# Kernel optimization log

Measured on AMD Instinct MI355X. Metric: run time of the kernel, lower is better.

The kernel has to match this reference:

```python
import jax, jax.numpy as jnp
import numpy as np

C = 256      # in_channels
CI = 128     # inter_channels = in_channels // 2
B, H, W = 16, 64, 64
EPS = 1e-5   # BatchNorm2d default eps


def conv1x1(x, w, b=None):
    # x: (b,c,h,w), w: (o,c) -> (b,o,h,w)
    out = jnp.einsum('bchw,oc->bohw', x, w)
    if b is not None:
        out = out + b[None, :, None, None]
    return out


def maxpool2x2(x):
    b, c, h, w = x.shape
    return x.reshape(b, c, h // 2, 2, w // 2, 2).max(axis=(3, 5))


def setup_inputs() -> dict:
    key = jax.random.key(0)
    ks = jax.random.split(key, 12)
    s_in = 1.0 / np.sqrt(C)
    s_int = 1.0 / np.sqrt(CI)
    return {
        'x': jax.random.normal(ks[0], (B, C, H, W), jnp.float32),
        'y': jax.random.normal(ks[1], (B, C, H, W), jnp.float32),
        'theta_w': jax.random.uniform(ks[2], (CI, C), jnp.float32, -s_in, s_in),
        'theta_b': jax.random.uniform(ks[3], (CI,), jnp.float32, -s_in, s_in),
        'phi_w': jax.random.uniform(ks[4], (CI, C), jnp.float32, -s_in, s_in),
        'phi_b': jax.random.uniform(ks[5], (CI,), jnp.float32, -s_in, s_in),
        'g_w': jax.random.uniform(ks[6], (CI, C), jnp.float32, -s_in, s_in),
        'g_b': jax.random.uniform(ks[7], (CI,), jnp.float32, -s_in, s_in),
        'W_w': jax.random.uniform(ks[8], (C, CI), jnp.float32, -s_int, s_int),
        'W_b': jax.random.uniform(ks[9], (C,), jnp.float32, -s_int, s_int),
        'bn_gamma': jax.random.normal(ks[10], (C,), jnp.float32) * 0.1,
        'bn_beta': jax.random.normal(ks[11], (C,), jnp.float32) * 0.1,
    }


def reference(x, y, theta_w, theta_b, phi_w, phi_b, g_w, g_b, W_w, W_b, bn_gamma, bn_beta):
    b, c, h, w = x.shape
    # g branch: 1x1 conv on y + 2x2 maxpool -> (b, CI, hw/4) -> (b, hw/4, CI)
    g_y = maxpool2x2(conv1x1(y, g_w, g_b)).reshape(b, CI, -1).transpose(0, 2, 1)
    # theta branch: 1x1 conv on x -> (b, hw, CI)
    theta_x = conv1x1(x, theta_w, theta_b).reshape(b, CI, -1).transpose(0, 2, 1)
    # phi branch: 1x1 conv on y + maxpool -> (b, CI, hw/4)
    phi_y = maxpool2x2(conv1x1(y, phi_w, phi_b)).reshape(b, CI, -1)
    # attention: (b, hw, hw/4)
    f = jnp.einsum('bnc,bcm->bnm', theta_x, phi_y)
    f_div_C = jax.nn.softmax(f, axis=-1)
    # z: (b, hw, CI) -> (b, CI, h, w)
    z = jnp.einsum('bnm,bmc->bnc', f_div_C, g_y)
    z = z.transpose(0, 2, 1).reshape(b, CI, h, w)
    # W: 1x1 conv + BatchNorm2d (training-mode batch stats, biased var)
    wz = conv1x1(z, W_w, W_b)
    mean = wz.mean(axis=(0, 2, 3), keepdims=True)
    var = wz.var(axis=(0, 2, 3), keepdims=True)
    wz = (wz - mean) * jax.lax.rsqrt(var + EPS)
    wz = wz * bn_gamma[None, :, None, None] + bn_beta[None, :, None, None]
    return wz + x
```

## Files before the change

kernel.cpp:

```cpp
#include <hip/hip_runtime.h>
#include <cstdint>

#define HW 4096
#define NC 256
#define CI 128
#define NB 16
#define MP 1024

typedef __bf16 bfv8 __attribute__((ext_vector_type(8)));
typedef float f32x16 __attribute__((ext_vector_type(16)));

__device__ __forceinline__ uint32_t bfr(float x) {
    uint32_t u = __float_as_uint(x);
    return (u + 0x7fffu + ((u >> 16) & 1u)) >> 16;
}
__device__ __forceinline__ uint32_t pkbf(float a, float b) {
    return bfr(a) | (bfr(b) << 16);
}
__device__ __forceinline__ float b2f_lo(uint32_t u) { return __uint_as_float(u << 16); }
__device__ __forceinline__ float b2f_hi(uint32_t u) { return __uint_as_float(u & 0xffff0000u); }

__global__ void k_castw(const float* __restrict__ a, const float* __restrict__ b,
                        const float* __restrict__ c, const float* __restrict__ d,
                        ushort* __restrict__ dst) {
    const float* srcs[4] = {a, b, c, d};
    const float* s = srcs[blockIdx.y];
    int i = (blockIdx.x * 256 + threadIdx.x) * 8;
    float4 v0 = *(const float4*)(s + i);
    float4 v1 = *(const float4*)(s + i + 4);
    uint4 o;
    o.x = pkbf(v0.x, v0.y); o.y = pkbf(v0.z, v0.w);
    o.z = pkbf(v1.x, v1.y); o.w = pkbf(v1.z, v1.w);
    *(uint4*)(dst + (size_t)blockIdx.y * 32768 + i) = o;
}

template<int O_TILE, int NT>
__global__ __launch_bounds__(256) void k_conv_mfma(
        const float* __restrict__ in, const ushort* __restrict__ wbf,
        const float* __restrict__ bias0, const float* __restrict__ bias1,
        ushort* __restrict__ outT) {
    __shared__ ushort xs[NT * 256];
    const int t = threadIdx.x;
    constexpr int tilesPerB = 4096 / NT;
    const int b = blockIdx.x / tilesPerB;
    const int n0 = (blockIdx.x % tilesPerB) * NT;
    const float* inb = in + ((size_t)b * 256) * 4096 + n0;

    constexpr int RPP = 1024 / NT;
    const int c0 = t % RPP, q = t / RPP;
    #pragma unroll
    for (int p = 0; p < 256 / RPP; p++) {
        int c = c0 + p * RPP;
        float4 v = *(const float4*)(inb + (size_t)c * 4096 + q * 4);
        #pragma unroll
        for (int j = 0; j < 4; j++) {
            int n = q * 4 + j;
            xs[n * 256 + (c ^ ((n & 7) << 3))] = (ushort)bfr((&v.x)[j]);
        }
    }
    __syncthreads();

    const int lane = t & 63, w = t >> 6;
    const int ln = lane & 31, hi = lane >> 5;
    int ob0, nb0;
    if (O_TILE == 256) { ob0 = w * 2; nb0 = 0; }
    else               { ob0 = (w & 1) * 2; nb0 = (w >> 1) * 2; }

    f32x16 acc[2][2];
    #pragma unroll
    for (int i = 0; i < 2; i++)
        #pragma unroll
        for (int j = 0; j < 2; j++)
            #pragma unroll
            for (int k = 0; k < 16; k++) acc[i][j][k] = 0.f;

    const ushort* wr0 = wbf + (size_t)(ob0 * 32 + ln) * 256 + hi * 8;
    const ushort* wr1 = wr0 + 32 * 256;
    const int nr0 = nb0 * 32 + ln, nr1 = nr0 + 32;
    const int sw0 = (nr0 & 7) << 3, sw1 = (nr1 & 7) << 3;

    #pragma unroll 4
    for (int ks = 0; ks < 16; ks++) {
        int k = ks * 16 + hi * 8;
        bfv8 wf0 = *(const bfv8*)(wr0 + ks * 16);
        bfv8 wf1 = *(const bfv8*)(wr1 + ks * 16);
        bfv8 x0 = *(const bfv8*)&xs[nr0 * 256 + (k ^ sw0)];
        bfv8 x1 = *(const bfv8*)&xs[nr1 * 256 + (k ^ sw1)];
        acc[0][0] = __builtin_amdgcn_mfma_f32_32x32x16_bf16(wf0, x0, acc[0][0], 0, 0, 0);
        acc[0][1] = __builtin_amdgcn_mfma_f32_32x32x16_bf16(wf0, x1, acc[0][1], 0, 0, 0);
        acc[1][0] = __builtin_amdgcn_mfma_f32_32x32x16_bf16(wf1, x0, acc[1][0], 0, 0, 0);
        acc[1][1] = __builtin_amdgcn_mfma_f32_32x32x16_bf16(wf1, x1, acc[1][1], 0, 0, 0);
    }

    #pragma unroll
    for (int oi = 0; oi < 2; oi++) {
        int obb = (ob0 + oi) * 32;
        #pragma unroll
        for (int grp = 0; grp < 4; grp++) {
            int og = obb + grp * 8 + hi * 4;
            const float* bp = (O_TILE == 256 && og >= 128) ? bias1 : bias0;
            float4 bv = *(const float4*)&bp[og & 127];
            #pragma unroll
            for (int ni = 0; ni < 2; ni++) {
                int n = n0 + (nb0 + ni) * 32 + ln;
                float r0 = acc[oi][ni][grp * 4 + 0] + bv.x;
                float r1 = acc[oi][ni][grp * 4 + 1] + bv.y;
                float r2 = acc[oi][ni][grp * 4 + 2] + bv.z;
                float r3 = acc[oi][ni][grp * 4 + 3] + bv.w;
                uint2 pk;
                pk.x = pkbf(r0, r1); pk.y = pkbf(r2, r3);
                *(uint2*)&outT[((size_t)b * 4096 + n) * O_TILE + og] = pk;
            }
        }
    }
}

__global__ __launch_bounds__(512) void k_convpool(
        const float* __restrict__ in, const ushort* __restrict__ wbf,
        const float* __restrict__ bias0, const float* __restrict__ bias1,
        ushort* __restrict__ phiT, ushort* __restrict__ gout) {
    __shared__ char lds[65536];
    ushort* xs = (ushort*)lds;
    const int t = threadIdx.x;
    const int b = blockIdx.x >> 5;
    const int r = blockIdx.x & 31;
    const int n0 = r * 128;
    const float* inb = in + ((size_t)b * 256) * 4096 + n0;

    {
        const int c0 = t & 7, qq = t >> 3;
        const int ch = qq >> 5, n4 = (qq & 31) * 4;
        #pragma unroll
        for (int p = 0; p < 16; p++) {
            int c = c0 + ch * 8 + p * 16;
            float4 v = *(const float4*)(inb + (size_t)c * 4096 + n4);
            #pragma unroll
            for (int j = 0; j < 4; j++) {
                int n = n4 + j;
                xs[n * 256 + (c ^ ((n & 7) << 3))] = (ushort)bfr((&v.x)[j]);
            }
        }
    }
    __syncthreads();

    const int lane = t & 63, w = t >> 6;
    const int ln = lane & 31, hi = lane >> 5;
    const int ob0 = (w & 3) * 2;
    const int nb0 = (w >> 2) * 2;
    const int lr = nb0 >> 1;

    f32x16 acc[2][2];
    #pragma unroll
    for (int i = 0; i < 2; i++)
        #pragma unroll
        for (int j = 0; j < 2; j++)
            #pragma unroll
            for (int k = 0; k < 16; k++) acc[i][j][k] = 0.f;

    const ushort* wr0 = wbf + (size_t)(ob0 * 32 + ln) * 256 + hi * 8;
    const ushort* wr1 = wr0 + 32 * 256;
    const int nr0 = nb0 * 32 + ln, nr1 = nr0 + 32;
    const int sw0 = (nr0 & 7) << 3, sw1 = (nr1 & 7) << 3;

    #pragma unroll 4
    for (int ks = 0; ks < 16; ks++) {
        int k = ks * 16 + hi * 8;
        bfv8 wf0 = *(const bfv8*)(wr0 + ks * 16);
        bfv8 wf1 = *(const bfv8*)(wr1 + ks * 16);
        bfv8 x0 = *(const bfv8*)&xs[nr0 * 256 + (k ^ sw0)];
        bfv8 x1 = *(const bfv8*)&xs[nr1 * 256 + (k ^ sw1)];
        acc[0][0] = __builtin_amdgcn_mfma_f32_32x32x16_bf16(wf0, x0, acc[0][0], 0, 0, 0);
        acc[0][1] = __builtin_amdgcn_mfma_f32_32x32x16_bf16(wf0, x1, acc[0][1], 0, 0, 0);
        acc[1][0] = __builtin_amdgcn_mfma_f32_32x32x16_bf16(wf1, x0, acc[1][0], 0, 0, 0);
        acc[1][1] = __builtin_amdgcn_mfma_f32_32x32x16_bf16(wf1, x1, acc[1][1], 0, 0, 0);
    }

    __syncthreads();
    float* poolreg = (float*)lds + lr * 8192;

    #pragma unroll
    for (int oi = 0; oi < 2; oi++) {
        #pragma unroll
        for (int grp = 0; grp < 4; grp++) {
            int og = (ob0 + oi) * 32 + grp * 8 + hi * 4;
            const float* bp = (og >= 128) ? bias1 : bias0;
            float4 bv = *(const float4*)&bp[og & 127];
            #pragma unroll
            for (int ni = 0; ni < 2; ni++) {
                #pragma unroll
                for (int j = 0; j < 4; j++) {
                    float v = acc[oi][ni][grp * 4 + j] + (&bv.x)[j];
                    float hm = fmaxf(v, __shfl_xor(v, 1, 64));
                    if ((ln & 1) == 0) {
                        int o = og + j;
                        poolreg[(o << 5) + ni * 16 + (ln >> 1)] = hm;
                    }
                }
            }
        }
    }
    __syncthreads();

    const float* p0 = (const float*)lds;
    const float* p1 = (const float*)lds + 8192;
    {
        int m = t >> 4, ci8 = (t & 15) * 8;
        uint32_t pk4[4];
        #pragma unroll
        for (int jp = 0; jp < 4; jp++) {
            int o0 = ci8 + jp * 2;
            float f0 = fmaxf(p0[(o0 << 5) + m], p1[(o0 << 5) + m]);
            float f1 = fmaxf(p0[((o0 + 1) << 5) + m], p1[((o0 + 1) << 5) + m]);
            pk4[jp] = pkbf(f0, f1);
        }
        *(uint4*)&phiT[((size_t)b * MP + r * 32 + m) * CI + ci8] =
            make_uint4(pk4[0], pk4[1], pk4[2], pk4[3]);
    }
    {
        int ci = t >> 2, mq = (t & 3) * 8;
        int o = 128 + ci;
        uint32_t pk4[4];
        #pragma unroll
        for (int jp = 0; jp < 4; jp++) {
            int mm = mq + jp * 2;
            float f0 = fmaxf(p0[(o << 5) + mm], p1[(o << 5) + mm]);
            float f1 = fmaxf(p0[(o << 5) + mm + 1], p1[(o << 5) + mm + 1]);
            pk4[jp] = pkbf(f0, f1);
        }
        *(uint4*)&gout[((size_t)b * CI + ci) * MP + r * 32 + mq] =
            make_uint4(pk4[0], pk4[1], pk4[2], pk4[3]);
    }
}

__global__ __launch_bounds__(512, 2) void k_attn_mfma(
        const ushort* __restrict__ thetaT, const ushort* __restrict__ phiT,
        const ushort* __restrict__ gmat, ushort* __restrict__ zout) {
    __shared__ char lds[65536];
    const int t = threadIdx.x;
    const int w = t >> 6, lane = t & 63;
    const int nq = lane & 31, hi = lane >> 5;
    const int ngrp = w & 3, h = w >> 2;
    const int b = blockIdx.x >> 5;
    const int q0 = (blockIdx.x & 31) << 7;

    {
        int row = t >> 2, s0 = (t & 3) * 4;
        const uint4* src = (const uint4*)(thetaT + ((size_t)b * HW + q0 + row) * CI) + s0;
        uint4* dstrow = (uint4*)(lds + row * 256);
        int rsw = row & 15;
        #pragma unroll
        for (int j = 0; j < 4; j++) {
            uint4 v = src[j];
            dstrow[(s0 + j) ^ rsw] = v;
        }
    }
    __syncthreads();
    bfv8 qf[8];
    {
        int row = ngrp * 32 + nq;
        int rsw = row & 15;
        #pragma unroll
        for (int ks = 0; ks < 8; ks++) {
            qf[ks] = *(const bfv8*)(lds + row * 256 + (((ks * 2 + hi) ^ rsw) << 4));
        }
    }
    __syncthreads();

    f32x16 zacc[4];
    #pragma unroll
    for (int ct = 0; ct < 4; ct++)
        #pragma unroll
        for (int i = 0; i < 16; i++) zacc[ct][i] = 0.f;
    float run_sum = 0.f;

    const int reg_r = t >> 7, tt = t & 127;
    const int hh = reg_r >> 1, kind = reg_r & 1;

    const char* phiB = lds + h * 32768;
    const char* gB   = lds + h * 32768 + 16384;
    const int rswp = nq & 15;
    const int rswg = nq & 7;

    for (int it = 0; it < 8; it++) {
        if (kind == 0) {
            int row = tt >> 1, s0 = (tt & 1) * 8;
            const uint4* src = (const uint4*)(phiT + ((size_t)b * MP + hh * 512 + it * 64 + row) * CI) + s0;
            uint4* dstrow = (uint4*)(lds + hh * 32768 + row * 256);
            int rsw = row & 15;
            #pragma unroll
            for (int j = 0; j < 8; j++) {
                uint4 v = src[j];
                dstrow[(s0 + j) ^ rsw] = v;
            }
        } else {
            int row = tt;
            const uint4* src = (const uint4*)(gmat + ((size_t)b * CI + row) * MP + hh * 512 + it * 64);
            uint4* dstrow = (uint4*)(lds + hh * 32768 + 16384 + row * 128);
            int rsw = row & 7;
            #pragma unroll
            for (int j = 0; j < 8; j++) {
                uint4 v = src[j];
                dstrow[j ^ rsw] = v;
            }
        }
        __syncthreads();

        f32x16 sA, sB;
        #pragma unroll
        for (int i = 0; i < 16; i++) { sA[i] = 0.f; sB[i] = 0.f; }
        __builtin_amdgcn_s_setprio(1);
        #pragma unroll
        for (int ks = 0; ks < 8; ks++) {
            int slot = ks * 2 + hi;
            bfv8 a0 = *(const bfv8*)(phiB + nq * 256 + ((slot ^ rswp) << 4));
            bfv8 a1 = *(const bfv8*)(phiB + (32 + nq) * 256 + ((slot ^ rswp) << 4));
            sA = __builtin_amdgcn_mfma_f32_32x32x16_bf16(a0, qf[ks], sA, 0, 0, 0);
            sB = __builtin_amdgcn_mfma_f32_32x32x16_bf16(a1, qf[ks], sB, 0, 0, 0);
        }
        __builtin_amdgcn_s_setprio(0);

        float pA[16], pB[16];
        #pragma unroll
        for (int i = 0; i < 16; i++) { pA[i] = __expf(sA[i]); run_sum += pA[i]; }
        #pragma unroll
        for (int i = 0; i < 16; i++) { pB[i] = __expf(sB[i]); run_sum += pB[i]; }

        uint32_t wA[8], wB[8], tA[8], tB[8];
        #pragma unroll
        for (int j = 0; j < 8; j++) { wA[j] = pkbf(pA[2 * j], pA[2 * j + 1]); wB[j] = pkbf(pB[2 * j], pB[2 * j + 1]); }
        #pragma unroll
        for (int j = 0; j < 8; j++) { tA[j] = (uint32_t)__shfl_xor((int)wA[j], 32, 64); tB[j] = (uint32_t)__shfl_xor((int)wB[j], 32, 64); }
        bool lo = (hi == 0);
        union PU { uint32_t u[4]; bfv8 v; } p0A, p1A, p0B, p1B;
        p0A.u[0] = lo ? wA[0] : tA[2]; p0A.u[1] = lo ? wA[1] : tA[3];
        p0A.u[2] = lo ? tA[0] : wA[2]; p0A.u[3] = lo ? tA[1] : wA[3];
        p1A.u[0] = lo ? wA[4] : tA[6]; p1A.u[1] = lo ? wA[5] : tA[7];
        p1A.u[2] = lo ? tA[4] : wA[6]; p1A.u[3] = lo ? tA[5] : wA[7];
        p0B.u[0] = lo ? wB[0] : tB[2]; p0B.u[1] = lo ? wB[1] : tB[3];
        p0B.u[2] = lo ? tB[0] : wB[2]; p0B.u[3] = lo ? tB[1] : wB[3];
        p1B.u[0] = lo ? wB[4] : tB[6]; p1B.u[1] = lo ? wB[5] : tB[7];
        p1B.u[2] = lo ? tB[4] : wB[6]; p1B.u[3] = lo ? tB[5] : wB[7];

        __builtin_amdgcn_s_setprio(1);
        #pragma unroll
        for (int ct = 0; ct < 4; ct++) {
            const char* grow = gB + (ct * 32 + nq) * 128;
            bfv8 g0 = *(const bfv8*)(grow + (((0 * 2 + hi) ^ rswg) << 4));
            bfv8 g1 = *(const bfv8*)(grow + (((1 * 2 + hi) ^ rswg) << 4));
            bfv8 g2 = *(const bfv8*)(grow + (((2 * 2 + hi) ^ rswg) << 4));
            bfv8 g3 = *(const bfv8*)(grow + (((3 * 2 + hi) ^ rswg) << 4));
            zacc[ct] = __builtin_amdgcn_mfma_f32_32x32x16_bf16(g0, p0A.v, zacc[ct], 0, 0, 0);
            zacc[ct] = __builtin_amdgcn_mfma_f32_32x32x16_bf16(g1, p1A.v, zacc[ct], 0, 0, 0);
            zacc[ct] = __builtin_amdgcn_mfma_f32_32x32x16_bf16(g2, p0B.v, zacc[ct], 0, 0, 0);
            zacc[ct] = __builtin_amdgcn_mfma_f32_32x32x16_bf16(g3, p1B.v, zacc[ct], 0, 0, 0);
        }
        __builtin_amdgcn_s_setprio(0);
        __syncthreads();
    }

    float pair_sum = run_sum + __shfl_xor(run_sum, 32, 64);
    float* ssum = (float*)(lds + 32768);
    if (hi == 0) ssum[w * 32 + nq] = pair_sum;
    __syncthreads();
    float psum = ssum[(w ^ 4) * 32 + nq];
    float rinv = 1.f / (pair_sum + psum);

    ushort* zr = zout + ((size_t)b * HW + q0 + ngrp * 32 + nq) * CI;
    const int rswz = nq & 15;
    #pragma unroll
    for (int pass = 0; pass < 2; pass++) {
        __syncthreads();
        if (h == 1) {
            #pragma unroll
            for (int cth = 0; cth < 2; cth++) {
                int ct = pass * 2 + cth;
                #pragma unroll
                for (int grp = 0; grp < 4; grp++) {
                    int slot = cth * 8 + grp * 2 + hi;
                    float4 v;
                    v.x = zacc[ct][grp * 4 + 0];
                    v.y = zacc[ct][grp * 4 + 1];
                    v.z = zacc[ct][grp * 4 + 2];
                    v.w = zacc[ct][grp * 4 + 3];
                    *(float4*)(lds + ngrp * 8192 + nq * 256 + ((slot ^ rswz) << 4)) = v;
                }
            }
        }
        __syncthreads();
        if (h == 0) {
            #pragma unroll
            for (int cth = 0; cth < 2; cth++) {
                int ct = pass * 2 + cth;
                #pragma unroll
                for (int grp = 0; grp < 4; grp++) {
                    int slot = cth * 8 + grp * 2 + hi;
                    float4 pv = *(const float4*)(lds + ngrp * 8192 + nq * 256 + ((slot ^ rswz) << 4));
                    float v0 = (zacc[ct][grp * 4 + 0] + pv.x) * rinv;
                    float v1 = (zacc[ct][grp * 4 + 1] + pv.y) * rinv;
                    float v2 = (zacc[ct][grp * 4 + 2] + pv.z) * rinv;
                    float v3 = (zacc[ct][grp * 4 + 3] + pv.w) * rinv;
                    int c0 = ct * 32 + grp * 8 + hi * 4;
                    uint2 pk;
                    pk.x = pkbf(v0, v1);
                    pk.y = pkbf(v2, v3);
                    *(uint2*)(zr + c0) = pk;
                }
            }
        }
    }
}

__global__ __launch_bounds__(256) void k_wz_mfma(
        const ushort* __restrict__ z, const ushort* __restrict__ Wbf,
        const float* __restrict__ Wb, ushort* __restrict__ wz,
        float* __restrict__ part) {
    __shared__ ushort zs[128 * 128];
    int t = threadIdx.x;
    int mtile = blockIdx.x;
    int oh = blockIdx.y;
    int b = mtile >> 5;
    int n0 = (mtile & 31) << 7;
    const ushort* zt = z + ((size_t)b * 4096 + n0) * 128;
    #pragma unroll
    for (int it = 0; it < 8; it++) {
        int d = (it * 256 + t) * 16;
        uint4 v = *(const uint4*)((const char*)zt + d);
        int n = d >> 8;
        int widx = (n << 7) + (((d & 255) ^ ((n & 7) << 4)) >> 1);
        *(uint4*)&zs[widx] = v;
    }
    __syncthreads();
    int lane = t & 63, w = t >> 6;
    int ln = lane & 31, hi = lane >> 5;
    int wr = w >> 1, wc = w & 1;
    f32x16 acc[2][2];
    #pragma unroll
    for (int i = 0; i < 2; i++)
        #pragma unroll
        for (int j = 0; j < 2; j++)
            #pragma unroll
            for (int k = 0; k < 16; k++) acc[i][j][k] = 0.f;
    const ushort* w0 = Wbf + (size_t)(oh * 128 + wc * 64 + ln) * 128 + hi * 8;
    const ushort* w1 = w0 + 32 * 128;
    int nr0 = wr * 64 + ln, nr1 = nr0 + 32;
    int sw0 = (nr0 & 7) << 3, sw1 = (nr1 & 7) << 3;
    #pragma unroll
    for (int ks = 0; ks < 8; ks++) {
        int k = ks * 16 + hi * 8;
        bfv8 a0 = *(const bfv8*)&zs[(nr0 << 7) + (k ^ sw0)];
        bfv8 a1 = *(const bfv8*)&zs[(nr1 << 7) + (k ^ sw1)];
        bfv8 b0 = *(const bfv8*)(w0 + ks * 16);
        bfv8 b1 = *(const bfv8*)(w1 + ks * 16);
        acc[0][0] = __builtin_amdgcn_mfma_f32_32x32x16_bf16(a0, b0, acc[0][0], 0, 0, 0);
        acc[0][1] = __builtin_amdgcn_mfma_f32_32x32x16_bf16(a0, b1, acc[0][1], 0, 0, 0);
        acc[1][0] = __builtin_amdgcn_mfma_f32_32x32x16_bf16(a1, b0, acc[1][0], 0, 0, 0);
        acc[1][1] = __builtin_amdgcn_mfma_f32_32x32x16_bf16(a1, b1, acc[1][1], 0, 0, 0);
    }
    #pragma unroll
    for (int obi = 0; obi < 2; obi++) {
        int o = oh * 128 + wc * 64 + obi * 32 + ln;
        float bv = Wb[o];
        ushort* orow = wz + ((size_t)b * 256 + o) * 4096 + n0;
        float s = 0.f, qq = 0.f;
        #pragma unroll
        for (int nbi = 0; nbi < 2; nbi++) {
            #pragma unroll
            for (int grp = 0; grp < 4; grp++) {
                float vals[4];
                #pragma unroll
                for (int j = 0; j < 4; j++) {
                    float v = acc[nbi][obi][grp * 4 + j] + bv;
                    vals[j] = v;
                    s += v; qq += v * v;
                }
                int n = (wr * 2 + nbi) * 32 + grp * 8 + hi * 4;
                uint2 pk;
                pk.x = pkbf(vals[0], vals[1]);
                pk.y = pkbf(vals[2], vals[3]);
                *(uint2*)(orow + n) = pk;
            }
        }
        s += __shfl_xor(s, 32, 64);
        qq += __shfl_xor(qq, 32, 64);
        if (hi == 0) {
            float* pr = part + (size_t)(mtile * 2 + wr) * 512;
            pr[o] = s;
            pr[256 + o] = qq;
        }
    }
}

__global__ __launch_bounds__(256) void k_bnstats(const float* __restrict__ part,
        const float* __restrict__ gamma, const float* __restrict__ beta,
        float* __restrict__ ss) {
    int o = blockIdx.x, t = threadIdx.x;
    float s = 0.f, q = 0.f;
    for (int k = t; k < 1024; k += 256) {
        s += part[(size_t)k * 512 + o];
        q += part[(size_t)k * 512 + 256 + o];
    }
    #pragma unroll
    for (int d = 32; d > 0; d >>= 1) { s += __shfl_down(s, d, 64); q += __shfl_down(q, d, 64); }
    __shared__ float rs[4], rq[4];
    int wave = t >> 6, lane = t & 63;
    if (lane == 0) { rs[wave] = s; rq[wave] = q; }
    __syncthreads();
    if (t == 0) {
        float S = rs[0] + rs[1] + rs[2] + rs[3];
        float Q = rq[0] + rq[1] + rq[2] + rq[3];
        const float inv = 1.0f / 65536.0f;
        float mean = S * inv;
        float var = Q * inv - mean * mean;
        float sc = gamma[o] * rsqrtf(var + 1e-5f);
        ss[o] = sc;
        ss[NC + o] = beta[o] - mean * sc;
    }
}

__global__ void k_apply(float* __restrict__ out, const ushort* __restrict__ wz,
        const float* __restrict__ x, const float* __restrict__ ss) {
    size_t i = ((size_t)blockIdx.x * 256 + threadIdx.x) * 8;
    int o = (int)((i >> 12) & 255);
    float sc = ss[o], sh = ss[NC + o];
    uint4 wv = *(const uint4*)(wz + i);
    float4 x0 = *(const float4*)(x + i);
    float4 x1 = *(const float4*)(x + i + 4);
    float4 r0, r1;
    r0.x = b2f_lo(wv.x) * sc + sh + x0.x;
    r0.y = b2f_hi(wv.x) * sc + sh + x0.y;
    r0.z = b2f_lo(wv.y) * sc + sh + x0.z;
    r0.w = b2f_hi(wv.y) * sc + sh + x0.w;
    r1.x = b2f_lo(wv.z) * sc + sh + x1.x;
    r1.y = b2f_hi(wv.z) * sc + sh + x1.y;
    r1.z = b2f_lo(wv.w) * sc + sh + x1.z;
    r1.w = b2f_hi(wv.w) * sc + sh + x1.w;
    *(float4*)(out + i) = r0;
    *(float4*)(out + i + 4) = r1;
}

extern "C" void kernel_launch(void* const* d_in, const int* in_sizes, int n_in,
                              void* d_out, int out_size, void* d_ws, size_t ws_size,
                              hipStream_t stream) {
    const float* x       = (const float*)d_in[0];
    const float* y       = (const float*)d_in[1];
    const float* theta_w = (const float*)d_in[2];
    const float* theta_b = (const float*)d_in[3];
    const float* phi_w   = (const float*)d_in[4];
    const float* phi_b   = (const float*)d_in[5];
    const float* g_w     = (const float*)d_in[6];
    const float* g_b     = (const float*)d_in[7];
    const float* W_w     = (const float*)d_in[8];
    const float* W_b     = (const float*)d_in[9];
    const float* bn_g    = (const float*)d_in[10];
    const float* bn_b    = (const float*)d_in[11];
    float* ws  = (float*)d_ws;
    float* out = (float*)d_out;

    ushort* wbf    = (ushort*)ws;
    ushort* thetaT = (ushort*)(ws + 65536);
    ushort* wzbf   = (ushort*)(ws + 65536);
    ushort* zbuf   = (ushort*)(ws + 8454144);
    ushort* phiT   = (ushort*)(ws + 12648448);
    ushort* gbuf   = (ushort*)(ws + 13697024);
    float*  part   = ws + 14745600;
    float*  ss     = ws + 15269888;

    k_castw<<<dim3(16, 4), 256, 0, stream>>>(theta_w, phi_w, g_w, W_w, wbf);

    k_conv_mfma<128, 128><<<NB * 32, 256, 0, stream>>>(x, wbf, theta_b, theta_b, thetaT);
    k_convpool<<<NB * 32, 512, 0, stream>>>(y, wbf + 32768, phi_b, g_b, phiT, gbuf);

    k_attn_mfma<<<NB * 32, 512, 0, stream>>>(thetaT, phiT, gbuf, zbuf);

    k_wz_mfma<<<dim3(NB * 32, 2), 256, 0, stream>>>(zbuf, wbf + 98304, W_b, wzbf, part);
    k_bnstats<<<256, 256, 0, stream>>>(part, bn_g, bn_b, ss);
    k_apply<<<8192, 256, 0, stream>>>(out, wzbf, x, ss);
}
```

Measured before the change: 197.6 us.

## Restructure attention kernel: 256 queries per block, full-key loop with double-buffered prefetch

The attention kernel now gives each of 8 waves its own 32 query rows over all 1024 keys, instead of splitting keys across two wave halves. That split needed a cross-wave LDS reduction of the partial outputs and softmax sums at the end, which is now gone. Key and value tiles are double-buffered: the next tile's global loads are issued into registers before compute and written to the other LDS buffer afterward, so there is one barrier per iteration. This halves the grid to 256 blocks, fewer than two per CU on MI355X, and the register prefetch adds register pressure.

```diff
diff --git a/kernel.cpp b/kernel.cpp
--- a/kernel.cpp
+++ b/kernel.cpp
@@ -239,17 +239,16 @@
     const int t = threadIdx.x;
     const int w = t >> 6, lane = t & 63;
     const int nq = lane & 31, hi = lane >> 5;
-    const int ngrp = w & 3, h = w >> 2;
-    const int b = blockIdx.x >> 5;
-    const int q0 = (blockIdx.x & 31) << 7;
+    const int b = blockIdx.x >> 4;
+    const int q0 = (blockIdx.x & 15) << 8;
 
     {
-        int row = t >> 2, s0 = (t & 3) * 4;
+        int row = t >> 1, s0 = (t & 1) * 8;
         const uint4* src = (const uint4*)(thetaT + ((size_t)b * HW + q0 + row) * CI) + s0;
         uint4* dstrow = (uint4*)(lds + row * 256);
         int rsw = row & 15;
         #pragma unroll
-        for (int j = 0; j < 4; j++) {
+        for (int j = 0; j < 8; j++) {
             uint4 v = src[j];
             dstrow[(s0 + j) ^ rsw] = v;
         }
@@ -257,8 +256,8 @@
     __syncthreads();
     bfv8 qf[8];
     {
-        int row = ngrp * 32 + nq;
-        int rsw = row & 15;
+        int row = w * 32 + nq;
+        int rsw = nq & 15;
         #pragma unroll
         for (int ks = 0; ks < 8; ks++) {
             qf[ks] = *(const bfv8*)(lds + row * 256 + (((ks * 2 + hi) ^ rsw) << 4));
@@ -273,37 +272,52 @@
         for (int i = 0; i < 16; i++) zacc[ct][i] = 0.f;
     float run_sum = 0.f;
 
-    const int reg_r = t >> 7, tt = t & 127;
-    const int hh = reg_r >> 1, kind = reg_r & 1;
-
-    const char* phiB = lds + h * 32768;
-    const char* gB   = lds + h * 32768 + 16384;
+    const int kind = t >> 8;
+    const int tt = t & 255;
+    const int prow = tt >> 2, ps0 = (tt & 3) * 4;
+    const int grow_i = tt >> 1, gs0 = (tt & 1) * 4;
+
     const int rswp = nq & 15;
     const int rswg = nq & 7;
 
-    for (int it = 0; it < 8; it++) {
+    auto issue_loads = [&](int it, uint4* pf) {
         if (kind == 0) {
-            int row = tt >> 1, s0 = (tt & 1) * 8;
-            const uint4* src = (const uint4*)(phiT + ((size_t)b * MP + hh * 512 + it * 64 + row) * CI) + s0;
-            uint4* dstrow = (uint4*)(lds + hh * 32768 + row * 256);
-            int rsw = row & 15;
-            #pragma unroll
-            for (int j = 0; j < 8; j++) {
-                uint4 v = src[j];
-                dstrow[(s0 + j) ^ rsw] = v;
-            }
+            const uint4* src = (const uint4*)(phiT + ((size_t)b * MP + it * 64 + prow) * CI) + ps0;
+            #pragma unroll
+            for (int j = 0; j < 4; j++) pf[j] = src[j];
         } else {
-            int row = tt;
-            const uint4* src = (const uint4*)(gmat + ((size_t)b * CI + row) * MP + hh * 512 + it * 64);
-            uint4* dstrow = (uint4*)(lds + hh * 32768 + 16384 + row * 128);
-            int rsw = row & 7;
-            #pragma unroll
-            for (int j = 0; j < 8; j++) {
-                uint4 v = src[j];
-                dstrow[j ^ rsw] = v;
-            }
-        }
-        __syncthreads();
+            const uint4* src = (const uint4*)(gmat + ((size_t)b * CI + grow_i) * MP + it * 64) + gs0;
+            #pragma unroll
+            for (int j = 0; j < 4; j++) pf[j] = src[j];
+        }
+    };
+    auto write_tile = [&](int buf, const uint4* pf) {
+        if (kind == 0) {
+            uint4* dstrow = (uint4*)(lds + buf * 32768 + prow * 256);
+            int rsw = prow & 15;
+            #pragma unroll
+            for (int j = 0; j < 4; j++) dstrow[(ps0 + j) ^ rsw] = pf[j];
+        } else {
+            uint4* dstrow = (uint4*)(lds + buf * 32768 + 16384 + grow_i * 128);
+            int rsw = grow_i & 7;
+            #pragma unroll
+            for (int j = 0; j < 4; j++) dstrow[(gs0 + j) ^ rsw] = pf[j];
+        }
+    };
+
+    {
+        uint4 pf[4];
+        issue_loads(0, pf);
+        write_tile(0, pf);
+    }
+    __syncthreads();
+
+    for (int it = 0; it < 16; it++) {
+        uint4 pf[4];
+        if (it < 15) issue_loads(it + 1, pf);
+
+        const char* phiB = lds + (it & 1) * 32768;
+        const char* gB   = phiB + 16384;
 
         f32x16 sA, sB;
         #pragma unroll
@@ -344,68 +358,34 @@
         __builtin_amdgcn_s_setprio(1);
         #pragma unroll
         for (int ct = 0; ct < 4; ct++) {
-            const char* grow = gB + (ct * 32 + nq) * 128;
-            bfv8 g0 = *(const bfv8*)(grow + (((0 * 2 + hi) ^ rswg) << 4));
-            bfv8 g1 = *(const bfv8*)(grow + (((1 * 2 + hi) ^ rswg) << 4));
-            bfv8 g2 = *(const bfv8*)(grow + (((2 * 2 + hi) ^ rswg) << 4));
-            bfv8 g3 = *(const bfv8*)(grow + (((3 * 2 + hi) ^ rswg) << 4));
+            const char* grw = gB + (ct * 32 + nq) * 128;
+            bfv8 g0 = *(const bfv8*)(grw + (((0 * 2 + hi) ^ rswg) << 4));
+            bfv8 g1 = *(const bfv8*)(grw + (((1 * 2 + hi) ^ rswg) << 4));
+            bfv8 g2 = *(const bfv8*)(grw + (((2 * 2 + hi) ^ rswg) << 4));
+            bfv8 g3 = *(const bfv8*)(grw + (((3 * 2 + hi) ^ rswg) << 4));
             zacc[ct] = __builtin_amdgcn_mfma_f32_32x32x16_bf16(g0, p0A.v, zacc[ct], 0, 0, 0);
             zacc[ct] = __builtin_amdgcn_mfma_f32_32x32x16_bf16(g1, p1A.v, zacc[ct], 0, 0, 0);
             zacc[ct] = __builtin_amdgcn_mfma_f32_32x32x16_bf16(g2, p0B.v, zacc[ct], 0, 0, 0);
             zacc[ct] = __builtin_amdgcn_mfma_f32_32x32x16_bf16(g3, p1B.v, zacc[ct], 0, 0, 0);
         }
         __builtin_amdgcn_s_setprio(0);
+
+        if (it < 15) write_tile((it + 1) & 1, pf);
         __syncthreads();
     }
 
     float pair_sum = run_sum + __shfl_xor(run_sum, 32, 64);
-    float* ssum = (float*)(lds + 32768);
-    if (hi == 0) ssum[w * 32 + nq] = pair_sum;
-    __syncthreads();
-    float psum = ssum[(w ^ 4) * 32 + nq];
-    float rinv = 1.f / (pair_sum + psum);
-
-    ushort* zr = zout + ((size_t)b * HW + q0 + ngrp * 32 + nq) * CI;
-    const int rswz = nq & 15;
-    #pragma unroll
-    for (int pass = 0; pass < 2; pass++) {
-        __syncthreads();
-        if (h == 1) {
-            #pragma unroll
-            for (int cth = 0; cth < 2; cth++) {
-                int ct = pass * 2 + cth;
-                #pragma unroll
-                for (int grp = 0; grp < 4; grp++) {
-                    int slot = cth * 8 + grp * 2 + hi;
-                    float4 v;
-                    v.x = zacc[ct][grp * 4 + 0];
-                    v.y = zacc[ct][grp * 4 + 1];
-                    v.z = zacc[ct][grp * 4 + 2];
-                    v.w = zacc[ct][grp * 4 + 3];
-                    *(float4*)(lds + ngrp * 8192 + nq * 256 + ((slot ^ rswz) << 4)) = v;
-                }
-            }
-        }
-        __syncthreads();
-        if (h == 0) {
-            #pragma unroll
-            for (int cth = 0; cth < 2; cth++) {
-                int ct = pass * 2 + cth;
-                #pragma unroll
-                for (int grp = 0; grp < 4; grp++) {
-                    int slot = cth * 8 + grp * 2 + hi;
-                    float4 pv = *(const float4*)(lds + ngrp * 8192 + nq * 256 + ((slot ^ rswz) << 4));
-                    float v0 = (zacc[ct][grp * 4 + 0] + pv.x) * rinv;
-                    float v1 = (zacc[ct][grp * 4 + 1] + pv.y) * rinv;
-                    float v2 = (zacc[ct][grp * 4 + 2] + pv.z) * rinv;
-                    float v3 = (zacc[ct][grp * 4 + 3] + pv.w) * rinv;
-                    int c0 = ct * 32 + grp * 8 + hi * 4;
-                    uint2 pk;
-                    pk.x = pkbf(v0, v1);
-                    pk.y = pkbf(v2, v3);
-                    *(uint2*)(zr + c0) = pk;
-                }
-            }
+    float rinv = 1.f / pair_sum;
+    ushort* zr = zout + ((size_t)b * HW + q0 + w * 32 + nq) * CI;
+    #pragma unroll
+    for (int ct = 0; ct < 4; ct++) {
+        #pragma unroll
+        for (int grp = 0; grp < 4; grp++) {
+            int c0 = ct * 32 + grp * 8 + hi * 4;
+            uint2 pk;
+            pk.x = pkbf(zacc[ct][grp * 4 + 0] * rinv, zacc[ct][grp * 4 + 1] * rinv);
+            pk.y = pkbf(zacc[ct][grp * 4 + 2] * rinv, zacc[ct][grp * 4 + 3] * rinv);
+            *(uint2*)(zr + c0) = pk;
         }
     }
 }
@@ -570,7 +550,7 @@
     k_conv_mfma<128, 128><<<NB * 32, 256, 0, stream>>>(x, wbf, theta_b, theta_b, thetaT);
     k_convpool<<<NB * 32, 512, 0, stream>>>(y, wbf + 32768, phi_b, g_b, phiT, gbuf);
 
-    k_attn_mfma<<<NB * 32, 512, 0, stream>>>(thetaT, phiT, gbuf, zbuf);
+    k_attn_mfma<<<NB * 16, 512, 0, stream>>>(thetaT, phiT, gbuf, zbuf);
 
     k_wz_mfma<<<dim3(NB * 32, 2), 256, 0, stream>>>(zbuf, wbf + 98304, W_b, wzbf, part);
     k_bnstats<<<256, 256, 0, stream>>>(part, bn_g, bn_b, ss);
```

Result: faster. 180.9 us (median of 4 runs) (-8.4%).
